# Kernel optimization log

Measured on AMD Instinct MI355X. Metric: run time of the kernel, lower is better.

The kernel has to match this reference:

```python
import jax, jax.numpy as jnp
import numpy as np

L = 16            # clip_len
STRIDES = (2, 2)
RADII = (0.15, 0.3)
NSAMPLES = (16, 32)
EPS = 1e-5
NEG_SLOPE = 0.2


def _fps(xyz, npoint):
    # furthest point sampling, xyz: (N, 3) -> (npoint,) int32 indices, start at 0
    N = xyz.shape[0]
    def step(carry, _):
        mind, last = carry
        d = jnp.sum((xyz - xyz[last]) ** 2, axis=-1)
        mind = jnp.minimum(mind, d)
        nxt = jnp.argmax(mind).astype(jnp.int32)
        return (mind, nxt), nxt
    _, rest = jax.lax.scan(step, (jnp.full((N,), 1e10, xyz.dtype), jnp.int32(0)), None, length=npoint - 1)
    return jnp.concatenate([jnp.zeros((1,), jnp.int32), rest])


def _shift_point(xyz, batch, N):
    # torch.roll(points, -1, dims=1) over the temporal axis, with last-frame extrapolation fix
    p = xyz.reshape(batch // L, L, N, 3)
    s = jnp.roll(p, -1, axis=1)
    shift_mean = jnp.mean(s[:, :-1] - p[:, :-1], axis=1)   # (Bc, N, 3)
    s = s.at[:, -1].set(p[:, -1] + shift_mean)
    return s.reshape(batch, N, 3)


def _conv_bn_lrelu(x, w, g, b):
    # 1x1 Conv2d (no bias) + GroupBN (per-channel over all other dims) + LeakyReLU(0.2)
    y = jnp.einsum('oc,bcnk->bonk', w, x)
    mu = jnp.mean(y, axis=(0, 2, 3), keepdims=True)
    var = jnp.var(y, axis=(0, 2, 3), keepdims=True)
    y = (y - mu) * jax.lax.rsqrt(var + EPS) * g[None, :, None, None] + b[None, :, None, None]
    return jnp.where(y > 0, y, NEG_SLOPE * y)


def _sa_module(xyz, features, stride, radius, nsample, layers):
    # xyz: (B, N, 3), features: (B, C, N)
    batch, N = xyz.shape[0], xyz.shape[1]
    q = _shift_point(xyz, batch, N)
    npoint = N // stride if stride > 1 else N
    if stride > 1:
        idx = jax.vmap(lambda p: _fps(p, npoint))(jax.lax.stop_gradient(q))  # (B, npoint)
        q = jax.vmap(lambda p, ix: p[ix])(q, idx)                            # (B, npoint, 3)
    # ball query: first `nsample` neighbors of each query within `radius`, padded with first hit
    d2 = jnp.sum((q[:, :, None, :] - xyz[:, None, :, :]) ** 2, axis=-1)      # (B, npoint, N)
    mask = d2 < radius * radius
    cand = jnp.where(mask, jnp.arange(N, dtype=jnp.int32)[None, None, :], N)
    srt = jnp.sort(cand, axis=-1)[..., :nsample]
    first = srt[..., :1]
    gidx = jnp.where(srt == N, first, srt)
    gidx = jnp.where(gidx == N, 0, gidx)                                     # fallback: no neighbor
    grouped_xyz = jax.vmap(lambda pts, ix: pts[ix])(xyz, gidx)               # (B, npoint, ns, 3)
    dp = (grouped_xyz - q[:, :, None, :]) / radius                           # normalize_dp
    dist = jnp.linalg.norm(dp, axis=-1)                                      # (B, npoint, ns) -> 4th grouped channel
    feats = jnp.swapaxes(features, 1, 2)                                     # (B, N, C)
    grouped_f = jax.vmap(lambda f, ix: f[ix])(feats, gidx)                   # (B, npoint, ns, C)
    x = jnp.concatenate([dp, grouped_f], axis=-1)                            # (B, npoint, ns, 3 + C)
    x = jnp.transpose(x, (0, 3, 1, 2))                                       # (B, 3 + C, npoint, ns)
    for (w, g, b) in layers:
        x = _conv_bn_lrelu(x, w, g, b)
    gate = jax.nn.sigmoid(dist)[:, None, :, :]                               # sigmoid(points[:, -1:])
    out = jnp.max(gate * x, axis=-1)                                         # (B, Cout, npoint)
    return q, out


def _forward(xyz, w1a, g1a, b1a, w1b, g1b, b1b, w2a, g2a, b2a, w2b, g2b, b2b):
    features = jnp.swapaxes(xyz, 1, 2)                                       # features default = xyz^T
    q1, f1 = _sa_module(xyz, features, STRIDES[0], RADII[0], NSAMPLES[0],
                        [(w1a, g1a, b1a), (w1b, g1b, b1b)])
    q2, f2 = _sa_module(q1, f1, STRIDES[1], RADII[1], NSAMPLES[1],
                        [(w2a, g2a, b2a), (w2b, g2b, b2b)])
    return f2                                                                # (32, 256, 128)


def setup_inputs() -> dict:
    key = jax.random.key(0)
    ks = jax.random.split(key, 5)
    B, N = 32, 512   # B = 2 clips * clip_len 16
    xyz = jax.random.uniform(ks[0], (B, N, 3), jnp.float32)
    def w(k, o, i):
        return jax.random.normal(k, (o, i), jnp.float32) / np.sqrt(i).astype(np.float32)
    return {
        'xyz': xyz,
        'w1a': w(ks[1], 64, 6),    'g1a': jnp.ones(64),  'b1a': jnp.zeros(64),
        'w1b': w(ks[2], 128, 64),  'g1b': jnp.ones(128), 'b1b': jnp.zeros(128),
        'w2a': w(ks[3], 128, 131), 'g2a': jnp.ones(128), 'b2a': jnp.zeros(128),
        'w2b': w(ks[4], 256, 128), 'g2b': jnp.ones(256), 'b2b': jnp.zeros(256),
    }


def reference(xyz, w1a, g1a, b1a, w1b, g1b, b1b, w2a, g2a, b2a, w2b, g2b, b2b):
    return _forward(xyz, w1a, g1a, b1a, w1b, g1b, b1b, w2a, g2a, b2a, w2b, g2b, b2b)
```

## Files before the change

kernel.cpp:

```cpp
#include <hip/hip_runtime.h>
#include <hip/hip_bf16.h>
#include <math.h>


#define BATCH 32
#define MCOLS 131072
#define CGRID 2048

typedef __attribute__((ext_vector_type(8))) short short8;
typedef __attribute__((ext_vector_type(4))) short short4v;
typedef __attribute__((ext_vector_type(4))) float f32x4;

__device__ __forceinline__ float b2f(short s) {
    return __uint_as_float(((unsigned)(unsigned short)s) << 16);
}
__device__ __forceinline__ short f2b(float f) {
    __hip_bfloat16 h = __float2bfloat16(f);
    return (short)__builtin_bit_cast(unsigned short, h);
}
__device__ __forceinline__ float dpp_row16_sum(float v) {
    int x;
    x = __builtin_amdgcn_update_dpp(0, __float_as_int(v), 0x111, 0xf, 0xf, true);
    v += __int_as_float(x);
    x = __builtin_amdgcn_update_dpp(0, __float_as_int(v), 0x112, 0xf, 0xf, true);
    v += __int_as_float(x);
    x = __builtin_amdgcn_update_dpp(0, __float_as_int(v), 0x114, 0xf, 0xf, true);
    v += __int_as_float(x);
    x = __builtin_amdgcn_update_dpp(0, __float_as_int(v), 0x118, 0xf, 0xf, true);
    v += __int_as_float(x);
    return v;
}
template<int C>
__device__ __forceinline__ float dpp_max(float v) {
    int x = __builtin_amdgcn_update_dpp(0, __float_as_int(v), C, 0xf, 0xf, true);
    return fmaxf(v, __int_as_float(x));
}
__device__ __forceinline__ float readlane_f(float v, int lane) {
    return __int_as_float(__builtin_amdgcn_readlane(__float_as_int(v), lane));
}

__global__ void prep_w(const float* __restrict__ w, int O, int C, int CK,
                       short* __restrict__ hi, short* __restrict__ lo) {
    int t = blockIdx.x * 256 + threadIdx.x;
    if (t >= O * CK) return;
    int o = t / CK, c = t % CK;
    float f = (c < C) ? w[o * C + c] : 0.f;
    short h = f2b(f);
    float fh = b2f(h);
    int NT = O >> 4;
    int ot = o >> 4, l15 = o & 15;
    int kc = c >> 5, quad = (c & 31) >> 3, j = c & 7;
    size_t idx = (((size_t)kc * NT + ot) * 64 + quad * 16 + l15) * 8 + j;
    hi[idx] = h;
    lo[idx] = f2b(f - fh);
}

template<int N, int NPOINT>
__global__ __launch_bounds__(64) void fps_kernel(const float* __restrict__ src,
                                                 float* __restrict__ qsel) {
    int b = blockIdx.x;
    int lane = threadIdx.x;
    int l = b & 15;
    constexpr int P = N / 64;
    __shared__ float4 qp[N];
    __shared__ int sel[NPOINT];
    if (l < 15) {
        const float* s = src + (size_t)(b + 1) * N * 3;
        for (int j = lane; j < N; j += 64)
            qp[j] = make_float4(s[j * 3 + 0], s[j * 3 + 1], s[j * 3 + 2], 0.f);
    } else {
        int g0 = b - 15;
        for (int j = lane; j < N; j += 64) {
            float v[3];
#pragma unroll
            for (int c = 0; c < 3; ++c) {
                float acc = 0.f;
                for (int i = 0; i < 15; ++i) {
                    float d = __fsub_rn(src[((size_t)(g0 + i + 1) * N + j) * 3 + c],
                                        src[((size_t)(g0 + i) * N + j) * 3 + c]);
                    acc = __fadd_rn(acc, d);
                }
                v[c] = __fadd_rn(src[((size_t)b * N + j) * 3 + c], __fdiv_rn(acc, 15.f));
            }
            qp[j] = make_float4(v[0], v[1], v[2], 0.f);
        }
    }
    if (lane == 0) sel[0] = 0;
    __syncthreads();
    float px[P], py[P], pz[P], mind[P];
#pragma unroll
    for (int p = 0; p < P; ++p) {
        float4 v = qp[lane * P + p];
        px[p] = v.x; py[p] = v.y; pz[p] = v.z;
        mind[p] = 1e10f;
    }
    float4 L0 = qp[0];
    float lx = L0.x, ly = L0.y, lz = L0.z;
    for (int s = 1; s < NPOINT; ++s) {
        float mn[P];
#pragma unroll
        for (int p = 0; p < P; ++p) {
            float dx = __fsub_rn(px[p], lx);
            float dy = __fsub_rn(py[p], ly);
            float dz = __fsub_rn(pz[p], lz);
            float d = __fadd_rn(__fadd_rn(__fmul_rn(dx, dx), __fmul_rn(dy, dy)),
                                __fmul_rn(dz, dz));
            float m2 = fminf(mind[p], d);
            mind[p] = m2;
            mn[p] = m2;
        }
        float t[P];
#pragma unroll
        for (int p = 0; p < P; ++p) t[p] = mn[p];
#pragma unroll
        for (int w = P / 2; w >= 1; w >>= 1)
#pragma unroll
            for (int p = 0; p < w; ++p) t[p] = fmaxf(t[p], t[p + w]);
        float local = t[0];
        float m = local;
        m = dpp_max<0x111>(m);
        m = dpp_max<0x112>(m);
        m = dpp_max<0x114>(m);
        m = dpp_max<0x118>(m);
        m = dpp_max<0x142>(m);
        m = dpp_max<0x143>(m);
        float maxd = readlane_f(m, 63);
        int enc = 0;
        float bx = px[0], by = py[0], bz = pz[0];
#pragma unroll
        for (int p = P - 1; p >= 1; --p) {
            bool e = (mn[p] == local);
            enc = e ? p : enc;
            bx = e ? px[p] : bx;
            by = e ? py[p] : by;
            bz = e ? pz[p] : bz;
        }
        bool e0 = (mn[0] == local);
        enc = e0 ? 0 : enc;
        bx = e0 ? px[0] : bx;
        by = e0 ? py[0] : by;
        bz = e0 ? pz[0] : bz;
        unsigned long long msk = __ballot(local == maxd);
        int winner = (int)__builtin_ctzll(msk);
        int last = winner * P + __builtin_amdgcn_readlane(enc, winner);
        lx = readlane_f(bx, winner);
        ly = readlane_f(by, winner);
        lz = readlane_f(bz, winner);
        if (lane == 0) sel[s] = last;
    }
    __syncthreads();
    for (int i = lane; i < NPOINT; i += 64) {
        float4 Pt = qp[sel[i]];
        size_t o = ((size_t)b * NPOINT + i) * 3;
        qsel[o + 0] = Pt.x;
        qsel[o + 1] = Pt.y;
        qsel[o + 2] = Pt.z;
    }
}

template<int N, int NPOINT, int NS, int CF, int CK>
__global__ __launch_bounds__(256) void ballq_kernel(
        const float* __restrict__ xyz,
        const float* __restrict__ qpts,
        const float* __restrict__ feats,
        float r2, float radius,
        short* __restrict__ X, float* __restrict__ gate) {
    static_assert((NS & (NS - 1)) == 0, "NS pow2");
    int lane = threadIdx.x & 63;
    int wib = threadIdx.x >> 6;
    int wid = blockIdx.x * 4 + wib;
    int b = wid / NPOINT;
    int i = wid % NPOINT;
    const float* qp = qpts + ((size_t)b * NPOINT + i) * 3;
    float qx = qp[0], qy = qp[1], qz = qp[2];
    __shared__ int gsh[4][NS];
    int* gidx = gsh[wib];
    int taken = 0, first = 0;
    bool any = false;
#pragma unroll
    for (int base = 0; base < N; base += 64) {
        int j = base + lane;
        const float* p = xyz + ((size_t)b * N + j) * 3;
        float dx = __fsub_rn(qx, p[0]);
        float dy = __fsub_rn(qy, p[1]);
        float dz = __fsub_rn(qz, p[2]);
        float d2 = __fadd_rn(__fadd_rn(__fmul_rn(dx, dx), __fmul_rn(dy, dy)),
                             __fmul_rn(dz, dz));
        bool in = d2 < r2;
        unsigned long long mk = __ballot(in);
        if (!any && mk) { first = base + __builtin_ctzll(mk); any = true; }
        int cb = __builtin_popcountll(mk & ((1ull << lane) - 1ull));
        int slot = taken + cb;
        if (in && slot < NS) gidx[slot] = j;
        taken += (int)__builtin_popcountll(mk);
    }
    if (taken < NS) {
        for (int s = taken + lane; s < NS; s += 64) gidx[s] = any ? first : 0;
    }
    __syncthreads();
    int m0 = (b * NPOINT + i) * NS;
    if (lane < NS) {
        int g = gidx[lane];
        const float* p = xyz + ((size_t)b * N + g) * 3;
        float dx = (p[0] - qx) / radius;
        float dy = (p[1] - qy) / radius;
        float dz = (p[2] - qz) / radius;
        float dist = sqrtf(dx * dx + dy * dy + dz * dz);
        gate[m0 + lane] = 1.f / (1.f + expf(-dist));
    }
    for (int e = lane; e < NS * CK; e += 64) {
        int s = e / CK;
        int c = e % CK;
        int g = gidx[s];
        float v;
        if (c < 3) {
            float qc = (c == 0) ? qx : ((c == 1) ? qy : qz);
            v = (xyz[((size_t)b * N + g) * 3 + c] - qc) / radius;
        } else if (c < 3 + CF) {
            v = feats[((size_t)b * N + g) * CF + (c - 3)];
        } else {
            v = 0.f;
        }
        X[(size_t)(m0 + s) * CK + c] = f2b(v);
    }
}

template<int CK, int O, bool AFF>
__global__ __launch_bounds__(256, 3) void mfma_conv(
        const short* __restrict__ X, const short* __restrict__ Whi,
        const short* __restrict__ Wlo, const float* __restrict__ ss,
        short* __restrict__ Y, float* __restrict__ pS, float* __restrict__ pS2) {
    constexpr int KC = CK / 32;
    constexpr int NT = O / 16;
    constexpr int OW = NT / 4;
    constexpr int LR = CK + 8;
    constexpr int CB = CK / 8;
    __shared__ __align__(16) short xs[64 * LR];
    __shared__ __align__(16) short wh[NT * 512];
    __shared__ __align__(16) short wl[NT * 512];
    __shared__ float ssl[AFF ? 2 * CK : 1];
    __shared__ float sblk[O], s2blk[O];
    int tid = threadIdx.x;
    int m0 = blockIdx.x * 64;

    if constexpr (AFF) {
        for (int i = tid; i < 2 * CK; i += 256) ssl[i] = ss[i];
        __syncthreads();
    }
    for (int idx = tid; idx < 64 * CB; idx += 256) {
        int r = idx / CB;
        int col = (idx % CB) * 8;
        short8 v = *(const short8*)(X + (size_t)(m0 + r) * CK + col);
        if constexpr (AFF) {
#pragma unroll
            for (int i = 0; i < 8; ++i) {
                float f = b2f(v[i]);
                f = fmaf(f, ssl[col + i], ssl[CK + col + i]);
                f = f > 0.f ? f : 0.2f * f;
                v[i] = f2b(f);
            }
        }
        *(short8*)(xs + r * LR + col) = v;
    }

    int lane = tid & 63;
    int wave = tid >> 6;
    int l15 = lane & 15;
    int quad = lane >> 4;
    int obase = wave * OW * 16;

    f32x4 acc[4][OW];
#pragma unroll
    for (int mt = 0; mt < 4; ++mt)
#pragma unroll
        for (int ot = 0; ot < OW; ++ot) acc[mt][ot] = (f32x4){0.f, 0.f, 0.f, 0.f};

    for (int kc = 0; kc < KC; ++kc) {
        __syncthreads();
        {
            const short8* gH = (const short8*)Whi + (size_t)kc * NT * 64;
            const short8* gL = (const short8*)Wlo + (size_t)kc * NT * 64;
            short8* lH = (short8*)wh;
            short8* lL = (short8*)wl;
            for (int i = tid; i < NT * 64; i += 256) { lH[i] = gH[i]; lL[i] = gL[i]; }
        }
        __syncthreads();
        short8 bf[4];
#pragma unroll
        for (int mt = 0; mt < 4; ++mt)
            bf[mt] = *(const short8*)(xs + (mt * 16 + l15) * LR + kc * 32 + quad * 8);
#pragma unroll
        for (int ot = 0; ot < OW; ++ot) {
            short8 ah = ((const short8*)wh)[(wave * OW + ot) * 64 + lane];
            short8 al = ((const short8*)wl)[(wave * OW + ot) * 64 + lane];
#pragma unroll
            for (int mt = 0; mt < 4; ++mt) {
                acc[mt][ot] = __builtin_amdgcn_mfma_f32_16x16x32_bf16(ah, bf[mt], acc[mt][ot], 0, 0, 0);
                acc[mt][ot] = __builtin_amdgcn_mfma_f32_16x16x32_bf16(al, bf[mt], acc[mt][ot], 0, 0, 0);
            }
        }
    }

#pragma unroll
    for (int mt = 0; mt < 4; ++mt) {
        size_t ybase = (size_t)(m0 + mt * 16 + l15) * O + obase + quad * 4;
#pragma unroll
        for (int ot = 0; ot < OW; ++ot) {
            short4v pk;
#pragma unroll
            for (int r4 = 0; r4 < 4; ++r4) pk[r4] = f2b(acc[mt][ot][r4]);
            *(short4v*)(Y + ybase + ot * 16) = pk;
        }
    }
#pragma unroll
    for (int ot = 0; ot < OW; ++ot) {
#pragma unroll
        for (int r4 = 0; r4 < 4; ++r4) {
            float s = 0.f, s2 = 0.f;
#pragma unroll
            for (int mt = 0; mt < 4; ++mt) {
                float v = acc[mt][ot][r4];
                s += v;
                s2 = fmaf(v, v, s2);
            }
            s = dpp_row16_sum(s);
            s2 = dpp_row16_sum(s2);
            if (l15 == 15) {
                int o = obase + ot * 16 + quad * 4 + r4;
                sblk[o] = s;
                s2blk[o] = s2;
            }
        }
    }
    __syncthreads();
    for (int o = tid; o < O; o += 256) {
        pS [(size_t)o * CGRID + blockIdx.x] = sblk[o];
        pS2[(size_t)o * CGRID + blockIdx.x] = s2blk[o];
    }
}

template<int O>
__global__ __launch_bounds__(256) void stats_fin(
        const float* __restrict__ pS, const float* __restrict__ pS2,
        const float* __restrict__ gm, const float* __restrict__ bt,
        float* __restrict__ norm) {
    int o = blockIdx.x;
    float s = 0.f, s2 = 0.f;
    for (int p = threadIdx.x; p < CGRID; p += 256) {
        s += pS[(size_t)o * CGRID + p];
        s2 += pS2[(size_t)o * CGRID + p];
    }
#pragma unroll
    for (int off = 32; off >= 1; off >>= 1) {
        s  += __shfl_xor(s,  off, 64);
        s2 += __shfl_xor(s2, off, 64);
    }
    __shared__ float sh[8];
    int wid = threadIdx.x >> 6;
    if ((threadIdx.x & 63) == 0) { sh[wid] = s; sh[4 + wid] = s2; }
    __syncthreads();
    if (threadIdx.x == 0) {
        float S  = sh[0] + sh[1] + sh[2] + sh[3];
        float S2 = sh[4] + sh[5] + sh[6] + sh[7];
        const float invM = 1.f / (float)MCOLS;
        float mu = S * invM;
        float var = S2 * invM - mu * mu;
        float sc = gm[o] * rsqrtf(var + 1e-5f);
        norm[o] = sc;
        norm[O + o] = bt[o] - mu * sc;
    }
}

template<int NS, int NPOINT, int O>
__global__ __launch_bounds__(256) void pool1_kernel(
        const short* __restrict__ Y, const float* __restrict__ norm,
        const float* __restrict__ gate, float* __restrict__ out) {
    int t = blockIdx.x * 256 + threadIdx.x;
    int o = t % O;
    int n = (t / O) % NPOINT;
    int b = t / (O * NPOINT);
    int m0 = (b * NPOINT + n) * NS;
    float sc = norm[o], sf = norm[O + o];
    float best = -INFINITY;
#pragma unroll
    for (int k = 0; k < NS; ++k) {
        float v = fmaf(b2f(Y[(size_t)(m0 + k) * O + o]), sc, sf);
        v = v > 0.f ? v : 0.2f * v;
        best = fmaxf(best, gate[m0 + k] * v);
    }
    out[t] = best;
}

__global__ __launch_bounds__(256) void pool2_kernel(
        const short* __restrict__ Y, const float* __restrict__ norm,
        const float* __restrict__ gate, float* __restrict__ out) {
    constexpr int NS = 32, NPOINT = 128, O = 256;
    int b  = blockIdx.x >> 3;
    int oc = (blockIdx.x >> 1) & 3;
    int nc = blockIdx.x & 1;
    __shared__ float trans[64][65];
    int tid = threadIdx.x;
    for (int w = 0; w < 16; ++w) {
        int idx = w * 256 + tid;
        int o_l = idx & 63;
        int n_l = idx >> 6;
        int o = oc * 64 + o_l;
        int n = nc * 64 + n_l;
        int m0 = (b * NPOINT + n) * NS;
        float sc = norm[o], sf = norm[O + o];
        float best = -INFINITY;
#pragma unroll
        for (int k = 0; k < NS; ++k) {
            float v = fmaf(b2f(Y[(size_t)(m0 + k) * O + o]), sc, sf);
            v = v > 0.f ? v : 0.2f * v;
            best = fmaxf(best, gate[m0 + k] * v);
        }
        trans[o_l][n_l] = best;
    }
    __syncthreads();
    for (int w = 0; w < 16; ++w) {
        int idx = w * 256 + tid;
        int o_l = idx >> 6;
        int n_l = idx & 63;
        out[((size_t)b * O + oc * 64 + o_l) * NPOINT + nc * 64 + n_l] = trans[o_l][n_l];
    }
}

extern "C" void kernel_launch(void* const* d_in, const int* in_sizes, int n_in,
                              void* d_out, int out_size, void* d_ws, size_t ws_size,
                              hipStream_t stream) {
    const float* xyz = (const float*)d_in[0];
    const float* w1a = (const float*)d_in[1];
    const float* g1a = (const float*)d_in[2];
    const float* b1a = (const float*)d_in[3];
    const float* w1b = (const float*)d_in[4];
    const float* g1b = (const float*)d_in[5];
    const float* b1b = (const float*)d_in[6];
    const float* w2a = (const float*)d_in[7];
    const float* g2a = (const float*)d_in[8];
    const float* b2a = (const float*)d_in[9];
    const float* w2b = (const float*)d_in[10];
    const float* g2b = (const float*)d_in[11];
    const float* b2b = (const float*)d_in[12];

    char* ws = (char*)d_ws;
    constexpr size_t OFF_Q1C   = 0;
    constexpr size_t OFF_GATE1 = 98304;
    constexpr size_t OFF_Q2C   = 622592;
    constexpr size_t OFF_GATE2 = 671744;
    constexpr size_t OFF_NORM  = 1196032;
    constexpr size_t OFF_W     = 1204224;
    constexpr size_t OFF_PS    = 1499136;
    constexpr size_t OFF_PS2   = 3596288;
    constexpr size_t OFF_A     = 5693440;
    constexpr size_t OFF_B     = 39247872;
    constexpr size_t OFF_F1    = OFF_B + 41943040;

    float* q1c   = (float*)(ws + OFF_Q1C);
    float* gate1 = (float*)(ws + OFF_GATE1);
    float* q2c   = (float*)(ws + OFF_Q2C);
    float* gate2 = (float*)(ws + OFF_GATE2);
    float* n1a   = (float*)(ws + OFF_NORM);
    float* n1b   = (float*)(ws + OFF_NORM + 512);
    float* n2a   = (float*)(ws + OFF_NORM + 1536);
    float* n2b   = (float*)(ws + OFF_NORM + 2560);
    short* w1aH  = (short*)(ws + OFF_W);
    short* w1aL  = w1aH + 2048;
    short* w1bH  = w1aL + 2048;
    short* w1bL  = w1bH + 8192;
    short* w2aH  = w1bL + 8192;
    short* w2aL  = w2aH + 20480;
    short* w2bH  = w2aL + 20480;
    short* w2bL  = w2bH + 32768;
    float* pS    = (float*)(ws + OFF_PS);
    float* pS2   = (float*)(ws + OFF_PS2);

    char* A = ws + OFF_A;
    char* B = ws + OFF_B;
    short* X1  = (short*)A;
    short* Y1a = (short*)B;
    short* Y1b = (short*)A;
    short* X2  = (short*)B;
    short* Y2a = (short*)A;
    short* Y2b = (short*)B;
    float* f1  = (float*)(ws + OFF_F1);

    const float r2_1 = (float)(0.15 * 0.15);
    const float r2_2 = (float)(0.3 * 0.3);

    prep_w<<<8,   256, 0, stream>>>(w1a, 64, 6, 32, w1aH, w1aL);
    prep_w<<<32,  256, 0, stream>>>(w1b, 128, 64, 64, w1bH, w1bL);
    prep_w<<<80,  256, 0, stream>>>(w2a, 128, 131, 160, w2aH, w2aL);
    prep_w<<<128, 256, 0, stream>>>(w2b, 256, 128, 128, w2bH, w2bL);

    fps_kernel<512, 256><<<32, 64, 0, stream>>>(xyz, q1c);
    ballq_kernel<512, 256, 16, 3, 32><<<2048, 256, 0, stream>>>(
        xyz, q1c, xyz, r2_1, 0.15f, X1, gate1);
    mfma_conv<32, 64, false><<<CGRID, 256, 0, stream>>>(X1, w1aH, w1aL, nullptr, Y1a, pS, pS2);
    stats_fin<64><<<64, 256, 0, stream>>>(pS, pS2, g1a, b1a, n1a);
    mfma_conv<64, 128, true><<<CGRID, 256, 0, stream>>>(Y1a, w1bH, w1bL, n1a, Y1b, pS, pS2);
    stats_fin<128><<<128, 256, 0, stream>>>(pS, pS2, g1b, b1b, n1b);
    pool1_kernel<16, 256, 128><<<4096, 256, 0, stream>>>(Y1b, n1b, gate1, f1);

    fps_kernel<256, 128><<<32, 64, 0, stream>>>(q1c, q2c);
    ballq_kernel<256, 128, 32, 128, 160><<<1024, 256, 0, stream>>>(
        q1c, q2c, f1, r2_2, 0.3f, X2, gate2);
    mfma_conv<160, 128, false><<<CGRID, 256, 0, stream>>>(X2, w2aH, w2aL, nullptr, Y2a, pS, pS2);
    stats_fin<128><<<128, 256, 0, stream>>>(pS, pS2, g2a, b2a, n2a);
    mfma_conv<128, 256, true><<<CGRID, 256, 0, stream>>>(Y2a, w2bH, w2bL, n2a, Y2b, pS, pS2);
    stats_fin<256><<<256, 256, 0, stream>>>(pS, pS2, g2b, b2b, n2b);
    pool2_kernel<<<256, 256, 0, stream>>>(Y2b, n2b, gate2, (float*)d_out);
}
```

Baseline: 434.3 us.

## Fuse weight prep and temporal shift into setup kernels, vectorize gather stores

```diff
diff --git a/kernel.cpp b/kernel.cpp
--- a/kernel.cpp
+++ b/kernel.cpp
@@ -39,9 +39,9 @@
     return __int_as_float(__builtin_amdgcn_readlane(__float_as_int(v), lane));
 }
 
-__global__ void prep_w(const float* __restrict__ w, int O, int C, int CK,
-                       short* __restrict__ hi, short* __restrict__ lo) {
-    int t = blockIdx.x * 256 + threadIdx.x;
+__device__ __forceinline__ void prep_elem(const float* __restrict__ w, int O, int C,
+                                          int CK, short* __restrict__ hi,
+                                          short* __restrict__ lo, int t) {
     if (t >= O * CK) return;
     int o = t / CK, c = t % CK;
     float f = (c < C) ? w[o * C + c] : 0.f;
@@ -55,36 +55,57 @@
     lo[idx] = f2b(f - fh);
 }
 
+__device__ __forceinline__ void shift_elem(const float* __restrict__ xyz,
+                                           float* __restrict__ qout, int t, int N) {
+    int c = t % 3;
+    int n = (t / 3) % N;
+    int b = t / (3 * N);
+    int l = b & 15;
+    float v;
+    if (l < 15) {
+        v = xyz[((size_t)(b + 1) * N + n) * 3 + c];
+    } else {
+        int g0 = b - 15;
+        float acc = 0.f;
+        for (int i = 0; i < 15; ++i) {
+            float d = __fsub_rn(xyz[((size_t)(g0 + i + 1) * N + n) * 3 + c],
+                                xyz[((size_t)(g0 + i) * N + n) * 3 + c]);
+            acc = __fadd_rn(acc, d);
+        }
+        v = __fadd_rn(xyz[((size_t)b * N + n) * 3 + c], __fdiv_rn(acc, 15.f));
+    }
+    qout[t] = v;
+}
+
+__global__ __launch_bounds__(256) void setup_kernel(
+        const float* __restrict__ w1a, const float* __restrict__ w1b,
+        const float* __restrict__ w2a, const float* __restrict__ w2b,
+        const float* __restrict__ xyz, float* __restrict__ qs1,
+        short* w1aH, short* w1aL, short* w1bH, short* w1bL,
+        short* w2aH, short* w2aL, short* w2bH, short* w2bL) {
+    int bid = blockIdx.x;
+    int tid = threadIdx.x;
+    if (bid < 8)        prep_elem(w1a, 64, 6, 32,    w1aH, w1aL, bid * 256 + tid);
+    else if (bid < 40)  prep_elem(w1b, 128, 64, 64,  w1bH, w1bL, (bid - 8) * 256 + tid);
+    else if (bid < 120) prep_elem(w2a, 128, 131, 160, w2aH, w2aL, (bid - 40) * 256 + tid);
+    else if (bid < 248) prep_elem(w2b, 256, 128, 128, w2bH, w2bL, (bid - 120) * 256 + tid);
+    else {
+        int t = (bid - 248) * 256 + tid;
+        if (t < BATCH * 512 * 3) shift_elem(xyz, qs1, t, 512);
+    }
+}
+
 template<int N, int NPOINT>
-__global__ __launch_bounds__(64) void fps_kernel(const float* __restrict__ src,
+__global__ __launch_bounds__(64) void fps_kernel(const float* __restrict__ q,
                                                  float* __restrict__ qsel) {
     int b = blockIdx.x;
     int lane = threadIdx.x;
-    int l = b & 15;
     constexpr int P = N / 64;
     __shared__ float4 qp[N];
     __shared__ int sel[NPOINT];
-    if (l < 15) {
-        const float* s = src + (size_t)(b + 1) * N * 3;
-        for (int j = lane; j < N; j += 64)
-            qp[j] = make_float4(s[j * 3 + 0], s[j * 3 + 1], s[j * 3 + 2], 0.f);
-    } else {
-        int g0 = b - 15;
-        for (int j = lane; j < N; j += 64) {
-            float v[3];
-#pragma unroll
-            for (int c = 0; c < 3; ++c) {
-                float acc = 0.f;
-                for (int i = 0; i < 15; ++i) {
-                    float d = __fsub_rn(src[((size_t)(g0 + i + 1) * N + j) * 3 + c],
-                                        src[((size_t)(g0 + i) * N + j) * 3 + c]);
-                    acc = __fadd_rn(acc, d);
-                }
-                v[c] = __fadd_rn(src[((size_t)b * N + j) * 3 + c], __fdiv_rn(acc, 15.f));
-            }
-            qp[j] = make_float4(v[0], v[1], v[2], 0.f);
-        }
-    }
+    const float* qb = q + (size_t)b * N * 3;
+    for (int j = lane; j < N; j += 64)
+        qp[j] = make_float4(qb[j * 3 + 0], qb[j * 3 + 1], qb[j * 3 + 2], 0.f);
     if (lane == 0) sel[0] = 0;
     __syncthreads();
     float px[P], py[P], pz[P], mind[P];
@@ -125,21 +146,16 @@
         m = dpp_max<0x142>(m);
         m = dpp_max<0x143>(m);
         float maxd = readlane_f(m, 63);
-        int enc = 0;
-        float bx = px[0], by = py[0], bz = pz[0];
-#pragma unroll
-        for (int p = P - 1; p >= 1; --p) {
+        int enc = P - 1;
+        float bx = px[P - 1], by = py[P - 1], bz = pz[P - 1];
+#pragma unroll
+        for (int p = P - 2; p >= 0; --p) {
             bool e = (mn[p] == local);
             enc = e ? p : enc;
             bx = e ? px[p] : bx;
             by = e ? py[p] : by;
             bz = e ? pz[p] : bz;
         }
-        bool e0 = (mn[0] == local);
-        enc = e0 ? 0 : enc;
-        bx = e0 ? px[0] : bx;
-        by = e0 ? py[0] : by;
-        bz = e0 ? pz[0] : bz;
         unsigned long long msk = __ballot(local == maxd);
         int winner = (int)__builtin_ctzll(msk);
         int last = winner * P + __builtin_amdgcn_readlane(enc, winner);
@@ -166,6 +182,7 @@
         float r2, float radius,
         short* __restrict__ X, float* __restrict__ gate) {
     static_assert((NS & (NS - 1)) == 0, "NS pow2");
+    static_assert(CK % 8 == 0, "CK mult of 8");
     int lane = threadIdx.x & 63;
     int wib = threadIdx.x >> 6;
     int wid = blockIdx.x * 4 + wib;
@@ -208,20 +225,28 @@
         float dist = sqrtf(dx * dx + dy * dy + dz * dz);
         gate[m0 + lane] = 1.f / (1.f + expf(-dist));
     }
-    for (int e = lane; e < NS * CK; e += 64) {
-        int s = e / CK;
-        int c = e % CK;
+    for (int e8 = lane * 8; e8 < NS * CK; e8 += 64 * 8) {
+        int s = e8 / CK;
+        int c0 = e8 % CK;
         int g = gidx[s];
-        float v;
-        if (c < 3) {
-            float qc = (c == 0) ? qx : ((c == 1) ? qy : qz);
-            v = (xyz[((size_t)b * N + g) * 3 + c] - qc) / radius;
-        } else if (c < 3 + CF) {
-            v = feats[((size_t)b * N + g) * CF + (c - 3)];
-        } else {
-            v = 0.f;
-        }
-        X[(size_t)(m0 + s) * CK + c] = f2b(v);
+        const float* frow = feats + (size_t)(b * N + g) * CF;
+        const float* prow = xyz + ((size_t)b * N + g) * 3;
+        short8 v8;
+#pragma unroll
+        for (int ii = 0; ii < 8; ++ii) {
+            int c = c0 + ii;
+            float v;
+            if (c < 3) {
+                float qc = (c == 0) ? qx : ((c == 1) ? qy : qz);
+                v = (prow[c] - qc) / radius;
+            } else if (c < 3 + CF) {
+                v = frow[c - 3];
+            } else {
+                v = 0.f;
+            }
+            v8[ii] = f2b(v);
+        }
+        *(short8*)(X + (size_t)(m0 + s) * CK + c0) = v8;
     }
 }
 
@@ -238,7 +263,7 @@
     __shared__ __align__(16) short xs[64 * LR];
     __shared__ __align__(16) short wh[NT * 512];
     __shared__ __align__(16) short wl[NT * 512];
-    __shared__ float ssl[AFF ? 2 * CK : 1];
+    __shared__ float ssl[AFF ? 2 * CK : 2];
     __shared__ float sblk[O], s2blk[O];
     int tid = threadIdx.x;
     int m0 = blockIdx.x * 64;
@@ -371,10 +396,16 @@
     }
 }
 
-template<int NS, int NPOINT, int O>
-__global__ __launch_bounds__(256) void pool1_kernel(
+__global__ __launch_bounds__(256) void pool1_shift2_kernel(
         const short* __restrict__ Y, const float* __restrict__ norm,
-        const float* __restrict__ gate, float* __restrict__ out) {
+        const float* __restrict__ gate, float* __restrict__ out,
+        const float* __restrict__ q1c, float* __restrict__ qs2) {
+    constexpr int NS = 16, NPOINT = 256, O = 128;
+    if (blockIdx.x >= 4096) {
+        int t = (int)(blockIdx.x - 4096) * 256 + threadIdx.x;
+        if (t < BATCH * 256 * 3) shift_elem(q1c, qs2, t, 256);
+        return;
+    }
     int t = blockIdx.x * 256 + threadIdx.x;
     int o = t % O;
     int n = (t / O) % NPOINT;
@@ -474,6 +505,7 @@
     short* w2bL  = w2bH + 32768;
     float* pS    = (float*)(ws + OFF_PS);
     float* pS2   = (float*)(ws + OFF_PS2);
+    float* qs2   = (float*)(ws + OFF_PS);
 
     char* A = ws + OFF_A;
     char* B = ws + OFF_B;
@@ -483,26 +515,26 @@
     short* X2  = (short*)B;
     short* Y2a = (short*)A;
     short* Y2b = (short*)B;
+    float* qs1 = (float*)B;
     float* f1  = (float*)(ws + OFF_F1);
 
     const float r2_1 = (float)(0.15 * 0.15);
     const float r2_2 = (float)(0.3 * 0.3);
 
-    prep_w<<<8,   256, 0, stream>>>(w1a, 64, 6, 32, w1aH, w1aL);
-    prep_w<<<32,  256, 0, stream>>>(w1b, 128, 64, 64, w1bH, w1bL);
-    prep_w<<<80,  256, 0, stream>>>(w2a, 128, 131, 160, w2aH, w2aL);
-    prep_w<<<128, 256, 0, stream>>>(w2b, 256, 128, 128, w2bH, w2bL);
-
-    fps_kernel<512, 256><<<32, 64, 0, stream>>>(xyz, q1c);
+    setup_kernel<<<440, 256, 0, stream>>>(w1a, w1b, w2a, w2b, xyz, qs1,
+                                          w1aH, w1aL, w1bH, w1bL,
+                                          w2aH, w2aL, w2bH, w2bL);
+
+    fps_kernel<512, 256><<<32, 64, 0, stream>>>(qs1, q1c);
     ballq_kernel<512, 256, 16, 3, 32><<<2048, 256, 0, stream>>>(
         xyz, q1c, xyz, r2_1, 0.15f, X1, gate1);
     mfma_conv<32, 64, false><<<CGRID, 256, 0, stream>>>(X1, w1aH, w1aL, nullptr, Y1a, pS, pS2);
     stats_fin<64><<<64, 256, 0, stream>>>(pS, pS2, g1a, b1a, n1a);
     mfma_conv<64, 128, true><<<CGRID, 256, 0, stream>>>(Y1a, w1bH, w1bL, n1a, Y1b, pS, pS2);
     stats_fin<128><<<128, 256, 0, stream>>>(pS, pS2, g1b, b1b, n1b);
-    pool1_kernel<16, 256, 128><<<4096, 256, 0, stream>>>(Y1b, n1b, gate1, f1);
-
-    fps_kernel<256, 128><<<32, 64, 0, stream>>>(q1c, q2c);
+    pool1_shift2_kernel<<<4192, 256, 0, stream>>>(Y1b, n1b, gate1, f1, q1c, qs2);
+
+    fps_kernel<256, 128><<<32, 64, 0, stream>>>(qs2, q2c);
     ballq_kernel<256, 128, 32, 128, 160><<<1024, 256, 0, stream>>>(
         q1c, q2c, f1, r2_2, 0.3f, X2, gate2);
     mfma_conv<160, 128, false><<<CGRID, 256, 0, stream>>>(X2, w2aH, w2aL, nullptr, Y2a, pS, pS2);
```

After: 389.6 us. -10.3%, faster.
